# Kernel optimization log

Hardware: AMD Instinct MI355X
Metric: run time of the kernel (lower is better)

Reference implementation:

```python
import jax, jax.numpy as jnp
import numpy as np

B, N, DIM, H, DH = 2, 2048, 256, 8, 32
DIM_INNER = H * DH  # 256


def setup_inputs() -> dict:
    key = jax.random.key(0)
    ks = jax.random.split(key, 8)
    s = DIM ** -0.5  # keep activations / logits in a sane range
    return {
        "x_real": jax.random.normal(ks[0], (B, N, DIM), jnp.float32),
        "x_imag": jax.random.normal(ks[1], (B, N, DIM), jnp.float32),
        "wq_r": jax.random.normal(ks[2], (DIM, DIM_INNER), jnp.float32) * s,
        "wq_i": jax.random.normal(ks[3], (DIM, DIM_INNER), jnp.float32) * s,
        "wkv_r": jax.random.normal(ks[4], (DIM, 2 * DIM_INNER), jnp.float32) * s,
        "wkv_i": jax.random.normal(ks[5], (DIM, 2 * DIM_INNER), jnp.float32) * s,
        "wo_r": jax.random.normal(ks[6], (DIM_INNER, DIM), jnp.float32) * s,
        "wo_i": jax.random.normal(ks[7], (DIM_INNER, DIM), jnp.float32) * s,
    }


def _clin(xr, xi, wr, wi):
    # complex linear: (xr + i xi) @ (wr + i wi)
    return xr @ wr - xi @ wi, xr @ wi + xi @ wr


def _split_heads(t):
    b, n, _ = t.shape
    return t.reshape(b, n, H, DH).transpose(0, 2, 1, 3)  # b h n d


def _merge_heads(t):
    b, h, n, d = t.shape
    return t.transpose(0, 2, 1, 3).reshape(b, n, h * d)


def reference(x_real, x_imag, wq_r, wq_i, wkv_r, wkv_i, wo_r, wo_i):
    # complex projections
    qr, qi = _clin(x_real, x_imag, wq_r, wq_i)
    kvr, kvi = _clin(x_real, x_imag, wkv_r, wkv_i)
    kr, vr = jnp.split(kvr, 2, axis=-1)
    ki, vi = jnp.split(kvi, 2, axis=-1)
    qr, qi, kr, ki, vr, vi = map(_split_heads, (qr, qi, kr, ki, vr, vi))

    # complex_attention_complete (sec 3.2 eq 3): 4 real SDPA replicas.
    # q repeat '(c r b)' -> blocks [qr, qr, qi, qi]; k repeat '(r c b)' -> [kr, ki, kr, ki]
    scale = DH ** -0.5
    Q = jnp.stack([qr, qr, qi, qi])        # [4, b, h, n, d]
    K = jnp.stack([kr, ki, kr, ki])
    sim = jnp.einsum('rbhid,rbhjd->rbhij', Q, K) * scale
    A = jax.nn.softmax(sim, axis=-1)       # [4, b, h, n, n]

    av = lambda a, v: jnp.einsum('bhij,bhjd->bhid', a, v)
    # sign-recombine trick: indices [0,3,5,6 | 1,2,4,7], sign [[1,-1,-1,-1],[1,1,1,-1]]
    o_r = av(A[0], vr) - av(A[1], vi) - av(A[2], vi) - av(A[3], vr)
    o_i = av(A[0], vi) + av(A[1], vr) + av(A[2], vr) - av(A[3], vi)

    mr, mi = _merge_heads(o_r), _merge_heads(o_i)
    out_r, out_i = _clin(mr, mi, wo_r, wo_i)
    # real view of the complex output: [b, n, dim, 2]
    return jnp.stack([out_r, out_i], axis=-1)
```

## Files before the change

### kernel.cpp

```cpp
#include <hip/hip_runtime.h>
#include <hip/hip_bf16.h>
#include <math.h>

namespace {
constexpr int kB = 2, kN = 2048, kDim = 256, kH = 8, kDH = 32;
constexpr int kBH = kB * kH;
constexpr long kPlane = (long)kBH * kN * kDH;
constexpr float kQScaleL2 = 0.25506852552f;
}

typedef unsigned short u16;
typedef short short8 __attribute__((ext_vector_type(8)));
typedef short short4v __attribute__((ext_vector_type(4)));
typedef float floatx16 __attribute__((ext_vector_type(16)));
#define MFMA_BF16(a, b, c) __builtin_amdgcn_mfma_f32_32x32x16_bf16(a, b, c, 0, 0, 0)

__device__ inline u16 bf16b(float x) {
    union { float f; unsigned u; } c; c.f = x;
    unsigned r = c.u + 0x7FFFu + ((c.u >> 16) & 1u);
    return (u16)(r >> 16);
}
__device__ inline unsigned pack2(float x, float y) {
    return (unsigned)bf16b(x) | ((unsigned)bf16b(y) << 16);
}
__device__ inline unsigned packtr(float lo, float hi) {
    return __builtin_amdgcn_perm(__float_as_uint(hi), __float_as_uint(lo), 0x07060302u);
}
__device__ inline short8 mk8(const float* e) {
    union { unsigned u[4]; short8 s; } c;
    c.u[0] = packtr(e[0], e[1]);
    c.u[1] = packtr(e[2], e[3]);
    c.u[2] = packtr(e[4], e[5]);
    c.u[3] = packtr(e[6], e[7]);
    return c.s;
}

__global__ __launch_bounds__(256, 2) void prep_w(
    const float* __restrict__ wq_r, const float* __restrict__ wq_i,
    const float* __restrict__ wkv_r, const float* __restrict__ wkv_i,
    const float* __restrict__ wo_r, const float* __restrict__ wo_i,
    u16* __restrict__ Wbig, u16* __restrict__ WoT)
{
    const long base = ((long)blockIdx.x * 256 + threadIdx.x) * 4;
    if (base < 786432) {
        const int c = (int)(base >> 9);
        const int k = (int)(base & 511);
        const int g = c >> 8, d = c & 255;
        const bool hi = k >= 256;
        const int k2 = hi ? k - 256 : k;
        const float* src;
        float sgn = 1.f;
        int col, stride;
        if (g < 2) {
            stride = 256; col = d;
            if (g == 0) { src = hi ? wq_i : wq_r; if (hi) sgn = -1.f; }
            else        { src = hi ? wq_r : wq_i; }
            sgn *= kQScaleL2;
        } else {
            stride = 512;
            col = (g >= 4) ? d + 256 : d;
            if ((g & 1) == 0) { src = hi ? wkv_i : wkv_r; if (hi) sgn = -1.f; }
            else              { src = hi ? wkv_r : wkv_i; }
        }
        short4v v;
        #pragma unroll
        for (int j = 0; j < 4; ++j)
            v[j] = (short)bf16b(src[(long)(k2 + j) * stride + col] * sgn);
        *(short4v*)(Wbig + base) = v;
    } else {
        const long o = base - 786432;
        const int c = (int)(o >> 9);
        const int k = (int)(o & 511);
        const bool hi = k >= 256;
        const int k2 = hi ? k - 256 : k;
        const float* src;
        float sgn = 1.f;
        int col;
        if (c < 256) { col = c;       src = hi ? wo_i : wo_r; if (hi) sgn = -1.f; }
        else         { col = c - 256; src = hi ? wo_r : wo_i; }
        short4v v;
        #pragma unroll
        for (int j = 0; j < 4; ++j)
            v[j] = (short)bf16b(src[(long)(k2 + j) * 256 + col] * sgn);
        *(short4v*)(WoT + o) = v;
    }
}

__global__ __launch_bounds__(256, 2) void gemm_proj(
    const float* __restrict__ xr_g, const float* __restrict__ xi_g,
    const u16* __restrict__ BT,
    u16* __restrict__ qr, u16* __restrict__ qi, u16* __restrict__ kr,
    u16* __restrict__ ki, u16* __restrict__ vrT, u16* __restrict__ viT)
{
    __shared__ __align__(16) u16 sA[128 * 32];
    __shared__ __align__(16) u16 sB[128 * 32];
    const int tid = threadIdx.x;
    const int lane = tid & 63, l31 = lane & 31, lh = lane >> 5;
    const int w = tid >> 6, wrow = w & 1, wcol = w >> 1;
    const int srow = tid >> 2, sseg = tid & 3;
    const int n0 = blockIdx.x * 128, m0 = blockIdx.y * 128;

    floatx16 a00 = {0}, a01 = {0}, a10 = {0}, a11 = {0};

    for (int kt = 0; kt < 512; kt += 32) {
        __syncthreads();
        const float* xbase = (kt < 256) ? xr_g : xi_g;
        const int kc = (kt & 255) + sseg * 8;
        #pragma unroll
        for (int i = 0; i < 2; ++i) {
            const int r = srow + i * 64;
            {
                const float* src = xbase + (long)(m0 + r) * 256 + kc;
                const float4 f0 = *(const float4*)(src);
                const float4 f1 = *(const float4*)(src + 4);
                union { __hip_bfloat162 b[4]; short8 s; } cv;
                cv.b[0] = __float22bfloat162_rn(make_float2(f0.x, f0.y));
                cv.b[1] = __float22bfloat162_rn(make_float2(f0.z, f0.w));
                cv.b[2] = __float22bfloat162_rn(make_float2(f1.x, f1.y));
                cv.b[3] = __float22bfloat162_rn(make_float2(f1.z, f1.w));
                *(short8*)(sA + r * 32 + sseg * 8) = cv.s;
            }
            *(short8*)(sB + r * 32 + sseg * 8) =
                *(const short8*)(BT + (long)(n0 + r) * 512 + kt + sseg * 8);
        }
        __syncthreads();
        #pragma unroll
        for (int s = 0; s < 2; ++s) {
            const int ko = s * 16 + lh * 8;
            const short8 fa0 = *(const short8*)(sA + (wrow * 64 + l31) * 32 + ko);
            const short8 fa1 = *(const short8*)(sA + (wrow * 64 + 32 + l31) * 32 + ko);
            const short8 fb0 = *(const short8*)(sB + (wcol * 64 + l31) * 32 + ko);
            const short8 fb1 = *(const short8*)(sB + (wcol * 64 + 32 + l31) * 32 + ko);
            a00 = MFMA_BF16(fa0, fb0, a00);
            a01 = MFMA_BF16(fa0, fb1, a01);
            a10 = MFMA_BF16(fa1, fb0, a10);
            a11 = MFMA_BF16(fa1, fb1, a11);
        }
    }

    floatx16 accs[2][2] = {{a00, a01}, {a10, a11}};
    #pragma unroll
    for (int rt = 0; rt < 2; ++rt) {
        #pragma unroll
        for (int ct = 0; ct < 2; ++ct) {
            const int colb = n0 + wcol * 64 + ct * 32;
            const int g = colb >> 8;
            const int h = (colb & 255) >> 5;
            if (g < 4) {
                u16* pl = (g == 0) ? qr : (g == 1) ? qi : (g == 2) ? kr : ki;
                #pragma unroll
                for (int reg = 0; reg < 16; ++reg) {
                    const int row = m0 + wrow * 64 + rt * 32 + (reg & 3) + 8 * (reg >> 2) + 4 * lh;
                    const int b = row >> 11, nn = row & 2047;
                    pl[(((long)(b * 8 + h)) * 2048 + nn) * 32 + l31] = bf16b(accs[rt][ct][reg]);
                }
            } else {
                u16* pl = (g == 4) ? vrT : viT;
                #pragma unroll
                for (int reg = 0; reg < 16; ++reg) {
                    const int row = m0 + wrow * 64 + rt * 32 + (reg & 3) + 8 * (reg >> 2) + 4 * lh;
                    const int b = row >> 11, nn = row & 2047;
                    const int np = (nn & ~12) | ((nn & 4) << 1) | ((nn & 8) >> 1);
                    pl[(((long)(b * 8 + h)) * 32 + l31) * 2048 + np] = bf16b(accs[rt][ct][reg]);
                }
            }
        }
    }
}

__global__ __launch_bounds__(256, 2) void attn_kernel(
    const u16* __restrict__ qr_g, const u16* __restrict__ qi_g,
    const u16* __restrict__ kr_g, const u16* __restrict__ ki_g,
    const u16* __restrict__ vrT_g, const u16* __restrict__ viT_g,
    u16* __restrict__ xo)
{
    __shared__ __align__(16) u16 smem[2][2][2][64 * 40];

    const int tid = threadIdx.x;
    const int lane = tid & 63, l31 = lane & 31, lh = lane >> 5;
    const int w = tid >> 6, qtype = w & 1, jhalf = w >> 1;
    const int bh = blockIdx.y;
    const int i0 = blockIdx.x * 32;
    const long base = (long)bh * kN * kDH;

    const u16* qg = (qtype ? qi_g : qr_g) + base;
    short8 qB0, qB1;
    {
        const u16* qp = qg + (long)(i0 + l31) * kDH;
        qB0 = *(const short8*)(qp + lh * 8);
        qB1 = *(const short8*)(qp + 16 + lh * 8);
    }

    const int t128 = tid & 127;
    const int srow = t128 & 63;
    const int hs = t128 >> 6;
    const u16* kplane = ((srow < 32) ? kr_g : ki_g) + base;
    const u16* vplane = ((srow < 32) ? vrT_g : viT_g)
                      + ((long)bh * 32 + (srow & 31)) * kN;
    const int t0 = jhalf * 32;
    const u16* kptr = kplane + ((long)t0 * 32 + (srow & 31)) * kDH + hs * 16;
    const u16* vptr = vplane + (long)t0 * 32 + hs * 16;

    short8 kpre0 = *(const short8*)(kptr);
    short8 kpre1 = *(const short8*)(kptr + 8);
    short8 vpre0 = *(const short8*)(vptr);
    short8 vpre1 = *(const short8*)(vptr + 8);

    floatx16 U0r = {0}, U0i = {0}, U1r = {0}, U1i = {0};
    float la0a = 0.f, la0b = 0.f, la1a = 0.f, la1b = 0.f;

    for (int tt = 0; tt < 32; ++tt) {
        u16* bK = smem[jhalf][0][tt & 1];
        u16* bV = smem[jhalf][1][tt & 1];
        *(short8*)(bK + srow * 40 + hs * 16) = kpre0;
        *(short8*)(bK + srow * 40 + hs * 16 + 8) = kpre1;
        *(short8*)(bV + srow * 40 + hs * 16) = vpre0;
        *(short8*)(bV + srow * 40 + hs * 16 + 8) = vpre1;
        __syncthreads();
        if (tt < 31) {
            kpre0 = *(const short8*)(kptr + (long)(tt + 1) * 1024);
            kpre1 = *(const short8*)(kptr + (long)(tt + 1) * 1024 + 8);
            vpre0 = *(const short8*)(vptr + (tt + 1) * 32);
            vpre1 = *(const short8*)(vptr + (tt + 1) * 32 + 8);
        }

        const short8 ka0 = *(const short8*)(bK + l31 * 40 + lh * 8);
        const short8 ka1 = *(const short8*)(bK + l31 * 40 + 16 + lh * 8);
        const short8 kb0 = *(const short8*)(bK + (32 + l31) * 40 + lh * 8);
        const short8 kb1 = *(const short8*)(bK + (32 + l31) * 40 + 16 + lh * 8);
        floatx16 S0 = {0}, S1 = {0};
        S0 = MFMA_BF16(ka0, qB0, S0);
        S0 = MFMA_BF16(ka1, qB1, S0);
        S1 = MFMA_BF16(kb0, qB0, S1);
        S1 = MFMA_BF16(kb1, qB1, S1);

        float e0[16], e1[16];
        #pragma unroll
        for (int r = 0; r < 16; ++r) {
            e0[r] = __builtin_amdgcn_exp2f(S0[r]);
            if (r & 1) la0a += e0[r]; else la0b += e0[r];
        }
        #pragma unroll
        for (int r = 0; r < 16; ++r) {
            e1[r] = __builtin_amdgcn_exp2f(S1[r]);
            if (r & 1) la1a += e1[r]; else la1b += e1[r];
        }
        const short8 F0a = mk8(&e0[0]);
        const short8 F0b = mk8(&e0[8]);
        const short8 F1a = mk8(&e1[0]);
        const short8 F1b = mk8(&e1[8]);

        const short8 va0 = *(const short8*)(bV + l31 * 40 + lh * 8);
        const short8 va1 = *(const short8*)(bV + l31 * 40 + 16 + lh * 8);
        const short8 vb0 = *(const short8*)(bV + (32 + l31) * 40 + lh * 8);
        const short8 vb1 = *(const short8*)(bV + (32 + l31) * 40 + 16 + lh * 8);

        U0r = MFMA_BF16(va0, F0a, U0r);
        U0r = MFMA_BF16(va1, F0b, U0r);
        U0i = MFMA_BF16(vb0, F0a, U0i);
        U0i = MFMA_BF16(vb1, F0b, U0i);
        U1r = MFMA_BF16(va0, F1a, U1r);
        U1r = MFMA_BF16(va1, F1b, U1r);
        U1i = MFMA_BF16(vb0, F1a, U1i);
        U1i = MFMA_BF16(vb1, F1b, U1i);
    }

    float La0 = la0a + la0b;
    float La1 = la1a + la1b;
    La0 += __shfl_xor(La0, 32);
    La1 += __shfl_xor(La1, 32);

    __syncthreads();
    float* sLa = (float*)smem;
    float* sPo = (float*)((u16*)smem + 1024);
    sLa[(w * 2 + 0) * 64 + lane] = La0;
    sLa[(w * 2 + 1) * 64 + lane] = La1;
    __syncthreads();
    const int pw = w ^ 2;
    const float iL0 = 1.f / (La0 + sLa[(pw * 2 + 0) * 64 + lane]);
    const float iL1 = 1.f / (La1 + sLa[(pw * 2 + 1) * 64 + lane]);

    float po_r[16], po_i[16];
    #pragma unroll
    for (int r = 0; r < 16; ++r) {
        if (qtype == 0) {
            po_r[r] =  U0r[r] * iL0 - U1i[r] * iL1;
            po_i[r] =  U0i[r] * iL0 + U1r[r] * iL1;
        } else {
            po_r[r] = -U0i[r] * iL0 - U1r[r] * iL1;
            po_i[r] =  U0r[r] * iL0 - U1i[r] * iL1;
        }
    }

    if (w != 0) {
        float* dst = sPo + ((size_t)w * 64 + lane) * 33;
        #pragma unroll
        for (int g = 0; g < 4; ++g) {
            *(float4*)(dst + 4 * g) =
                make_float4(po_r[4 * g], po_r[4 * g + 1], po_r[4 * g + 2], po_r[4 * g + 3]);
            *(float4*)(dst + 16 + 4 * g) =
                make_float4(po_i[4 * g], po_i[4 * g + 1], po_i[4 * g + 2], po_i[4 * g + 3]);
        }
    }
    __syncthreads();
    if (w == 0) {
        #pragma unroll
        for (int pw2 = 1; pw2 < 4; ++pw2) {
            const float* src = sPo + ((size_t)pw2 * 64 + lane) * 33;
            #pragma unroll
            for (int g = 0; g < 4; ++g) {
                const float4 ar = *(const float4*)(src + 4 * g);
                const float4 ai = *(const float4*)(src + 16 + 4 * g);
                po_r[4 * g + 0] += ar.x; po_r[4 * g + 1] += ar.y;
                po_r[4 * g + 2] += ar.z; po_r[4 * g + 3] += ar.w;
                po_i[4 * g + 0] += ai.x; po_i[4 * g + 1] += ai.y;
                po_i[4 * g + 2] += ai.z; po_i[4 * g + 3] += ai.w;
            }
        }
        const int b = bh >> 3, h = bh & 7;
        u16* xrow = xo + ((long)(b * 2048) + i0 + l31) * 512 + h * 32;
        #pragma unroll
        for (int g = 0; g < 4; ++g) {
            const int d0 = 8 * g + 4 * lh;
            union { unsigned u[2]; uint2 v; } pr, pi;
            pr.u[0] = pack2(po_r[4 * g + 0], po_r[4 * g + 1]);
            pr.u[1] = pack2(po_r[4 * g + 2], po_r[4 * g + 3]);
            pi.u[0] = pack2(po_i[4 * g + 0], po_i[4 * g + 1]);
            pi.u[1] = pack2(po_i[4 * g + 2], po_i[4 * g + 3]);
            *(uint2*)(xrow + d0) = pr.v;
            *(uint2*)(xrow + 256 + d0) = pi.v;
        }
    }
}

__global__ __launch_bounds__(256, 2) void gemm_oproj(
    const u16* __restrict__ Xo, const u16* __restrict__ BT, float* __restrict__ out)
{
    __shared__ __align__(16) u16 sA[128 * 32];
    __shared__ __align__(16) u16 sB[128 * 32];
    const int tid = threadIdx.x;
    const int lane = tid & 63, l31 = lane & 31, lh = lane >> 5;
    const int w = tid >> 6, wrow = w & 1, wcol = w >> 1;
    const int srow = tid >> 2, sseg = tid & 3;
    const int n0 = blockIdx.x * 128, m0 = blockIdx.y * 128;

    floatx16 a00 = {0}, a01 = {0}, a10 = {0}, a11 = {0};

    for (int kt = 0; kt < 512; kt += 32) {
        __syncthreads();
        #pragma unroll
        for (int i = 0; i < 2; ++i) {
            const int r = srow + i * 64;
            *(short8*)(sA + r * 32 + sseg * 8) =
                *(const short8*)(Xo + (long)(m0 + r) * 512 + kt + sseg * 8);
            *(short8*)(sB + r * 32 + sseg * 8) =
                *(const short8*)(BT + (long)(n0 + r) * 512 + kt + sseg * 8);
        }
        __syncthreads();
        #pragma unroll
        for (int s = 0; s < 2; ++s) {
            const int ko = s * 16 + lh * 8;
            const short8 fa0 = *(const short8*)(sA + (wrow * 64 + l31) * 32 + ko);
            const short8 fa1 = *(const short8*)(sA + (wrow * 64 + 32 + l31) * 32 + ko);
            const short8 fb0 = *(const short8*)(sB + (wcol * 64 + l31) * 32 + ko);
            const short8 fb1 = *(const short8*)(sB + (wcol * 64 + 32 + l31) * 32 + ko);
            a00 = MFMA_BF16(fa0, fb0, a00);
            a01 = MFMA_BF16(fa0, fb1, a01);
            a10 = MFMA_BF16(fa1, fb0, a10);
            a11 = MFMA_BF16(fa1, fb1, a11);
        }
    }

    floatx16 accs[2][2] = {{a00, a01}, {a10, a11}};
    #pragma unroll
    for (int rt = 0; rt < 2; ++rt) {
        #pragma unroll
        for (int ct = 0; ct < 2; ++ct) {
            const int colb = n0 + wcol * 64 + ct * 32;
            #pragma unroll
            for (int reg = 0; reg < 16; ++reg) {
                const int row = m0 + wrow * 64 + rt * 32 + (reg & 3) + 8 * (reg >> 2) + 4 * lh;
                const int col = colb + l31;
                const float val = accs[rt][ct][reg];
                if (colb < 256) out[(long)row * 512 + col * 2] = val;
                else            out[(long)row * 512 + (col - 256) * 2 + 1] = val;
            }
        }
    }
}

extern "C" void kernel_launch(void* const* d_in, const int* in_sizes, int n_in,
                              void* d_out, int out_size, void* d_ws, size_t ws_size,
                              hipStream_t stream) {
    const float* xr    = (const float*)d_in[0];
    const float* xi    = (const float*)d_in[1];
    const float* wq_r  = (const float*)d_in[2];
    const float* wq_i  = (const float*)d_in[3];
    const float* wkv_r = (const float*)d_in[4];
    const float* wkv_i = (const float*)d_in[5];
    const float* wo_r  = (const float*)d_in[6];
    const float* wo_i  = (const float*)d_in[7];
    float* out = (float*)d_out;

    u16* ws16 = (u16*)d_ws;
    u16* qr   = ws16 + 0 * kPlane;
    u16* qi   = ws16 + 1 * kPlane;
    u16* kr   = ws16 + 2 * kPlane;
    u16* ki   = ws16 + 3 * kPlane;
    u16* vrT  = ws16 + 4 * kPlane;
    u16* viT  = ws16 + 5 * kPlane;
    u16* xo   = ws16 + 6 * kPlane;
    u16* Wbig = ws16 + 8 * kPlane;
    u16* WoT  = Wbig + 786432;

    prep_w<<<1024, 256, 0, stream>>>(wq_r, wq_i, wkv_r, wkv_i, wo_r, wo_i, Wbig, WoT);
    gemm_proj<<<dim3(12, 32), 256, 0, stream>>>(xr, xi, Wbig, qr, qi, kr, ki, vrT, viT);
    attn_kernel<<<dim3(kN / 32, kBH), 256, 0, stream>>>(qr, qi, kr, ki, vrT, viT, xo);
    gemm_oproj<<<dim3(4, 32), 256, 0, stream>>>(xo, WoT, out);
}
```

Before: 190.3 us.

## Widen attention block to 64 query rows with 8 waves sharing K/V tiles

The attention kernel now runs 512 threads (8 waves) per block covering 64 query rows in two 32-row strips, so each staged K/V shared-memory tile is reused by twice as many waves and global K/V traffic per query row is halved. The grid is transposed so blockIdx.x walks batch-heads, which changes the order blocks are scheduled and may improve L2 locality. The cross-wave reduction becomes a two-stage tree over the extra syncs. Launch bounds move to 512 threads with 4 minimum blocks, which constrains register allocation and could cause spills.

Result: no change. 192.4 us (+1.1%).

```diff
diff --git a/kernel.cpp b/kernel.cpp
--- a/kernel.cpp
+++ b/kernel.cpp
@@ -168,7 +168,7 @@
     }
 }
 
-__global__ __launch_bounds__(256, 2) void attn_kernel(
+__global__ __launch_bounds__(512, 4) void attn_kernel(
     const u16* __restrict__ qr_g, const u16* __restrict__ qi_g,
     const u16* __restrict__ kr_g, const u16* __restrict__ ki_g,
     const u16* __restrict__ vrT_g, const u16* __restrict__ viT_g,
@@ -178,33 +178,31 @@
 
     const int tid = threadIdx.x;
     const int lane = tid & 63, l31 = lane & 31, lh = lane >> 5;
-    const int w = tid >> 6, qtype = w & 1, jhalf = w >> 1;
-    const int bh = blockIdx.y;
-    const int i0 = blockIdx.x * 32;
+    const int w = tid >> 6;
+    const int strip = w & 1, qtype = (w >> 1) & 1, jhalf = w >> 2;
+    const int bh = blockIdx.x;
+    const int i0 = blockIdx.y * 64;
     const long base = (long)bh * kN * kDH;
 
     const u16* qg = (qtype ? qi_g : qr_g) + base;
     short8 qB0, qB1;
     {
-        const u16* qp = qg + (long)(i0 + l31) * kDH;
+        const u16* qp = qg + (long)(i0 + strip * 32 + l31) * kDH;
         qB0 = *(const short8*)(qp + lh * 8);
         qB1 = *(const short8*)(qp + 16 + lh * 8);
     }
 
-    const int t128 = tid & 127;
-    const int srow = t128 & 63;
-    const int hs = t128 >> 6;
-    const u16* kplane = ((srow < 32) ? kr_g : ki_g) + base;
-    const u16* vplane = ((srow < 32) ? vrT_g : viT_g)
-                      + ((long)bh * 32 + (srow & 31)) * kN;
+    const int t256 = tid & 255;
+    const int srow = t256 & 63;
+    const int sseg = t256 >> 6;
     const int t0 = jhalf * 32;
-    const u16* kptr = kplane + ((long)t0 * 32 + (srow & 31)) * kDH + hs * 16;
-    const u16* vptr = vplane + (long)t0 * 32 + hs * 16;
-
-    short8 kpre0 = *(const short8*)(kptr);
-    short8 kpre1 = *(const short8*)(kptr + 8);
-    short8 vpre0 = *(const short8*)(vptr);
-    short8 vpre1 = *(const short8*)(vptr + 8);
+    const u16* kptr = ((srow < 32) ? kr_g : ki_g) + base
+                    + ((long)t0 * 32 + (srow & 31)) * kDH + sseg * 8;
+    const u16* vptr = ((srow < 32) ? vrT_g : viT_g)
+                    + ((long)bh * 32 + (srow & 31)) * kN + (long)t0 * 32 + sseg * 8;
+
+    short8 kreg = *(const short8*)kptr;
+    short8 vreg = *(const short8*)vptr;
 
     floatx16 U0r = {0}, U0i = {0}, U1r = {0}, U1i = {0};
     float la0a = 0.f, la0b = 0.f, la1a = 0.f, la1b = 0.f;
@@ -212,16 +210,12 @@
     for (int tt = 0; tt < 32; ++tt) {
         u16* bK = smem[jhalf][0][tt & 1];
         u16* bV = smem[jhalf][1][tt & 1];
-        *(short8*)(bK + srow * 40 + hs * 16) = kpre0;
-        *(short8*)(bK + srow * 40 + hs * 16 + 8) = kpre1;
-        *(short8*)(bV + srow * 40 + hs * 16) = vpre0;
-        *(short8*)(bV + srow * 40 + hs * 16 + 8) = vpre1;
+        *(short8*)(bK + srow * 40 + sseg * 8) = kreg;
+        *(short8*)(bV + srow * 40 + sseg * 8) = vreg;
         __syncthreads();
         if (tt < 31) {
-            kpre0 = *(const short8*)(kptr + (long)(tt + 1) * 1024);
-            kpre1 = *(const short8*)(kptr + (long)(tt + 1) * 1024 + 8);
-            vpre0 = *(const short8*)(vptr + (tt + 1) * 32);
-            vpre1 = *(const short8*)(vptr + (tt + 1) * 32 + 8);
+            kreg = *(const short8*)(kptr + (long)(tt + 1) * 1024);
+            vreg = *(const short8*)(vptr + (tt + 1) * 32);
         }
 
         const short8 ka0 = *(const short8*)(bK + l31 * 40 + lh * 8);
@@ -272,11 +266,11 @@
 
     __syncthreads();
     float* sLa = (float*)smem;
-    float* sPo = (float*)((u16*)smem + 1024);
+    float* sPo = (float*)((u16*)smem + 2048);
     sLa[(w * 2 + 0) * 64 + lane] = La0;
     sLa[(w * 2 + 1) * 64 + lane] = La1;
     __syncthreads();
-    const int pw = w ^ 2;
+    const int pw = w ^ 4;
     const float iL0 = 1.f / (La0 + sLa[(pw * 2 + 0) * 64 + lane]);
     const float iL1 = 1.f / (La1 + sLa[(pw * 2 + 1) * 64 + lane]);
 
@@ -292,8 +286,8 @@
         }
     }
 
-    if (w != 0) {
-        float* dst = sPo + ((size_t)w * 64 + lane) * 33;
+    if (jhalf == 1) {
+        float* dst = sPo + ((size_t)(w - 4) * 64 + lane) * 33;
         #pragma unroll
         for (int g = 0; g < 4; ++g) {
             *(float4*)(dst + 4 * g) =
@@ -303,22 +297,43 @@
         }
     }
     __syncthreads();
-    if (w == 0) {
-        #pragma unroll
-        for (int pw2 = 1; pw2 < 4; ++pw2) {
-            const float* src = sPo + ((size_t)pw2 * 64 + lane) * 33;
-            #pragma unroll
-            for (int g = 0; g < 4; ++g) {
-                const float4 ar = *(const float4*)(src + 4 * g);
-                const float4 ai = *(const float4*)(src + 16 + 4 * g);
-                po_r[4 * g + 0] += ar.x; po_r[4 * g + 1] += ar.y;
-                po_r[4 * g + 2] += ar.z; po_r[4 * g + 3] += ar.w;
-                po_i[4 * g + 0] += ai.x; po_i[4 * g + 1] += ai.y;
-                po_i[4 * g + 2] += ai.z; po_i[4 * g + 3] += ai.w;
-            }
+    if (jhalf == 0) {
+        const float* src = sPo + ((size_t)w * 64 + lane) * 33;
+        #pragma unroll
+        for (int g = 0; g < 4; ++g) {
+            const float4 ar = *(const float4*)(src + 4 * g);
+            const float4 ai = *(const float4*)(src + 16 + 4 * g);
+            po_r[4 * g + 0] += ar.x; po_r[4 * g + 1] += ar.y;
+            po_r[4 * g + 2] += ar.z; po_r[4 * g + 3] += ar.w;
+            po_i[4 * g + 0] += ai.x; po_i[4 * g + 1] += ai.y;
+            po_i[4 * g + 2] += ai.z; po_i[4 * g + 3] += ai.w;
+        }
+    }
+    __syncthreads();
+    if (jhalf == 0 && qtype == 1) {
+        float* dst = sPo + ((size_t)(w - 2) * 64 + lane) * 33;
+        #pragma unroll
+        for (int g = 0; g < 4; ++g) {
+            *(float4*)(dst + 4 * g) =
+                make_float4(po_r[4 * g], po_r[4 * g + 1], po_r[4 * g + 2], po_r[4 * g + 3]);
+            *(float4*)(dst + 16 + 4 * g) =
+                make_float4(po_i[4 * g], po_i[4 * g + 1], po_i[4 * g + 2], po_i[4 * g + 3]);
+        }
+    }
+    __syncthreads();
+    if (w < 2) {
+        const float* src = sPo + ((size_t)w * 64 + lane) * 33;
+        #pragma unroll
+        for (int g = 0; g < 4; ++g) {
+            const float4 ar = *(const float4*)(src + 4 * g);
+            const float4 ai = *(const float4*)(src + 16 + 4 * g);
+            po_r[4 * g + 0] += ar.x; po_r[4 * g + 1] += ar.y;
+            po_r[4 * g + 2] += ar.z; po_r[4 * g + 3] += ar.w;
+            po_i[4 * g + 0] += ai.x; po_i[4 * g + 1] += ai.y;
+            po_i[4 * g + 2] += ai.z; po_i[4 * g + 3] += ai.w;
         }
         const int b = bh >> 3, h = bh & 7;
-        u16* xrow = xo + ((long)(b * 2048) + i0 + l31) * 512 + h * 32;
+        u16* xrow = xo + ((long)(b * 2048) + i0 + strip * 32 + l31) * 512 + h * 32;
         #pragma unroll
         for (int g = 0; g < 4; ++g) {
             const int d0 = 8 * g + 4 * lh;
@@ -415,6 +430,6 @@
 
     prep_w<<<1024, 256, 0, stream>>>(wq_r, wq_i, wkv_r, wkv_i, wo_r, wo_i, Wbig, WoT);
     gemm_proj<<<dim3(12, 32), 256, 0, stream>>>(xr, xi, Wbig, qr, qi, kr, ki, vrT, viT);
-    attn_kernel<<<dim3(kN / 32, kBH), 256, 0, stream>>>(qr, qi, kr, ki, vrT, viT, xo);
+    attn_kernel<<<dim3(kBH, kN / 64), 512, 0, stream>>>(qr, qi, kr, ki, vrT, viT, xo);
     gemm_oproj<<<dim3(4, 32), 256, 0, stream>>>(xo, WoT, out);
 }
```
